# Optimization experiments

Hardware: AMD Instinct MI355X
Metric: run time of the kernel (lower is better)

## Reference

```python
import jax, jax.numpy as jnp
import numpy as np

EPS = 1e-6

def _phi(x):
    # elu(x) + 1 feature map
    return jax.nn.elu(x) + 1.0

def setup_inputs() -> dict:
    key = jax.random.key(0)
    kq, kk, kv = jax.random.split(key, 3)
    N, L, S, H, D, M = 8, 4096, 4096, 8, 64, 64
    queries = jax.random.normal(kq, (N, L, H, D), dtype=jnp.float32)
    keys = jax.random.normal(kk, (N, S, H, D), dtype=jnp.float32)
    values = jax.random.normal(kv, (N, S, H, M), dtype=jnp.float32)
    key_mask = jnp.ones((N, S), dtype=jnp.float32)  # key_lengths.float_matrix
    return {"queries": queries, "keys": keys, "values": values, "key_mask": key_mask}

def reference(queries, keys, values, key_mask):
    Q = _phi(queries)                                   # [N,L,H,D]
    K = _phi(keys) * key_mask[:, :, None, None]         # [N,S,H,D]
    KV = jnp.einsum('nshd,nshm->nhmd', K, values)       # [N,H,M,D]
    Z = 1.0 / (jnp.einsum('nlhd,nhd->nlh', Q, K.sum(axis=1)) + EPS)  # [N,L,H]
    V = jnp.einsum('nlhd,nhmd,nlh->nlhm', Q, KV, Z)     # [N,L,H,M]
    return V
```

## Files before the change

### kernel.cpp

```cpp
#include <hip/hip_runtime.h>


#define SLEN 4096
#define LLEN 4096
#define NHTOT 64
#define HD   512
#define NSPLIT 8
#define EPSF 1e-6f

typedef short s16x8 __attribute__((ext_vector_type(8)));
typedef float f32x4 __attribute__((ext_vector_type(4)));

__device__ __forceinline__ float phi(float x) {
    return x > 0.0f ? x + 1.0f : __expf(x);
}

__device__ __forceinline__ unsigned pack_hi2(float a, float b) {
    return (__float_as_uint(a) >> 16) | (__float_as_uint(b) & 0xFFFF0000u);
}
__device__ __forceinline__ float bres(float x) {
    return x - __uint_as_float(__float_as_uint(x) & 0xFFFF0000u);
}
__device__ __forceinline__ void bsplit(float x, short& hi, short& lo) {
    const unsigned bx = __float_as_uint(x);
    hi = (short)(bx >> 16);
    const float hf = __uint_as_float(bx & 0xFFFF0000u);
    lo = (short)(__float_as_uint(x - hf) >> 16);
}

__global__ __launch_bounds__(256, 2)
void la_phase1(const float* __restrict__ Kg, const float* __restrict__ Vg,
               const float* __restrict__ maskg,
               float* __restrict__ KVp, float* __restrict__ Ksump) {
    __shared__ float smem[4][4096];
    __shared__ float ksb[16 * 64];

    const int tid  = threadIdx.x;
    const int w    = tid >> 6;
    const int lane = tid & 63;
    const int nh   = blockIdx.y;
    const int n    = nh >> 3;
    const int h    = nh & 7;
    const int sp   = blockIdx.x;

    const int r  = lane & 15;
    const int a  = lane >> 4;
    const int c4 = r * 4;

    char* const wbase = (char*)&smem[w][0];
    char* const kthi = wbase;
    char* const ktlo = wbase + 4096;
    char* const vthi = wbase + 8192;
    char* const vtlo = wbase + 12288;

    const size_t base = (size_t)n * SLEN * HD + (size_t)h * 64;
    const float* mrow = maskg + (size_t)n * SLEN;
    const int wrow0 = sp * 512 + w * 128;

    const int woff0 = ((((a >> 1) ^ (r & 3)) << 4) | ((a & 1) << 3));
    const int rkey  = (r >> 2) & 3;

    f32x4 acc[4][4];
    #pragma unroll
    for (int i = 0; i < 4; ++i)
        #pragma unroll
        for (int j = 0; j < 4; ++j)
            acc[i][j] = (f32x4){0.f, 0.f, 0.f, 0.f};
    float4 ksp = make_float4(0.f, 0.f, 0.f, 0.f);

    float4 pk[2][4], pv[2][4];
    float  pm[2][4];
    #pragma unroll
    for (int u = 0; u < 2; ++u)
        #pragma unroll
        for (int j = 0; j < 4; ++j) {
            const int s = wrow0 + u * 16 + a * 4 + j;
            const size_t g = base + (size_t)s * HD + c4;
            pk[u][j] = *(const float4*)(Kg + g);
            pv[u][j] = *(const float4*)(Vg + g);
            pm[u][j] = mrow[s];
        }

    #pragma unroll
    for (int t = 0; t < 4; ++t) {
        #pragma unroll
        for (int u = 0; u < 2; ++u) {
            float4 kf[4];
            #pragma unroll
            for (int j = 0; j < 4; ++j) {
                float4 kq = pk[u][j];
                const float mm = pm[u][j];
                kq.x = phi(kq.x) * mm; kq.y = phi(kq.y) * mm;
                kq.z = phi(kq.z) * mm; kq.w = phi(kq.w) * mm;
                kf[j] = kq;
                ksp.x += kq.x; ksp.y += kq.y; ksp.z += kq.z; ksp.w += kq.w;
            }
            const int wo = woff0 ^ (u << 5);
            #pragma unroll
            for (int i = 0; i < 4; ++i) {
                const int doff = r * 256 + i * 64 + wo;
                const float k0 = (&kf[0].x)[i], k1 = (&kf[1].x)[i];
                const float k2 = (&kf[2].x)[i], k3 = (&kf[3].x)[i];
                *(uint2*)(kthi + doff) = make_uint2(pack_hi2(k0, k1), pack_hi2(k2, k3));
                *(uint2*)(ktlo + doff) = make_uint2(pack_hi2(bres(k0), bres(k1)),
                                                   pack_hi2(bres(k2), bres(k3)));
                const float v0 = (&pv[u][0].x)[i], v1 = (&pv[u][1].x)[i];
                const float v2 = (&pv[u][2].x)[i], v3 = (&pv[u][3].x)[i];
                *(uint2*)(vthi + doff) = make_uint2(pack_hi2(v0, v1), pack_hi2(v2, v3));
                *(uint2*)(vtlo + doff) = make_uint2(pack_hi2(bres(v0), bres(v1)),
                                                   pack_hi2(bres(v2), bres(v3)));
            }
        }
        if (t < 3) {
            #pragma unroll
            for (int u = 0; u < 2; ++u)
                #pragma unroll
                for (int j = 0; j < 4; ++j) {
                    const int s = wrow0 + (t + 1) * 32 + u * 16 + a * 4 + j;
                    const size_t g = base + (size_t)s * HD + c4;
                    pk[u][j] = *(const float4*)(Kg + g);
                    pv[u][j] = *(const float4*)(Vg + g);
                    pm[u][j] = mrow[s];
                }
        }
        s16x8 Ah[4], Al[4];
        const int cho = (a ^ rkey) << 4;
        #pragma unroll
        for (int dt = 0; dt < 4; ++dt) {
            const int off = dt * 1024 + r * 64 + cho;
            Ah[dt] = *(const s16x8*)(kthi + off);
            Al[dt] = *(const s16x8*)(ktlo + off);
        }
        #pragma unroll
        for (int mt = 0; mt < 4; ++mt) {
            const int off = mt * 1024 + r * 64 + cho;
            const s16x8 Bh = *(const s16x8*)(vthi + off);
            const s16x8 Bl = *(const s16x8*)(vtlo + off);
            #pragma unroll
            for (int dt = 0; dt < 4; ++dt) {
                acc[dt][mt] = __builtin_amdgcn_mfma_f32_16x16x32_bf16(Ah[dt], Bh, acc[dt][mt], 0, 0, 0);
                acc[dt][mt] = __builtin_amdgcn_mfma_f32_16x16x32_bf16(Ah[dt], Bl, acc[dt][mt], 0, 0, 0);
                acc[dt][mt] = __builtin_amdgcn_mfma_f32_16x16x32_bf16(Al[dt], Bh, acc[dt][mt], 0, 0, 0);
            }
        }
    }

    *(float4*)&ksb[(w * 4 + a) * 64 + c4] = ksp;

    float* pw = &smem[w][0];
    #pragma unroll
    for (int dt = 0; dt < 4; ++dt)
        #pragma unroll
        for (int mt = 0; mt < 4; ++mt)
            #pragma unroll
            for (int p = 0; p < 4; ++p)
                pw[(dt * 16 + a * 4 + p) * 64 + mt * 16 + r] = acc[dt][mt][p];
    __syncthreads();

    float* outp = KVp + ((size_t)sp * NHTOT + nh) * 4096;
    #pragma unroll
    for (int j = 0; j < 4; ++j) {
        const int f = (j * 256 + tid) * 4;
        float4 s0  = *(const float4*)&smem[0][f];
        const float4 b1 = *(const float4*)&smem[1][f];
        const float4 b2 = *(const float4*)&smem[2][f];
        const float4 b3 = *(const float4*)&smem[3][f];
        s0.x += b1.x + b2.x + b3.x;
        s0.y += b1.y + b2.y + b3.y;
        s0.z += b1.z + b2.z + b3.z;
        s0.w += b1.w + b2.w + b3.w;
        *(float4*)&outp[f] = s0;
    }
    if (tid < 64) {
        float ssum = 0.f;
        #pragma unroll
        for (int rr = 0; rr < 16; ++rr) ssum += ksb[rr * 64 + tid];
        Ksump[((size_t)sp * NHTOT + nh) * 64 + tid] = ssum;
    }
}

__global__ __launch_bounds__(256)
void la_reduce(const float* __restrict__ KVp, const float* __restrict__ Ksump,
               short* __restrict__ KVThi, short* __restrict__ KVTlo,
               float* __restrict__ Ksum) {
    __shared__ float ld[64 * 20];

    const int nh  = blockIdx.y;
    const int mb  = blockIdx.x * 16;
    const int tid = threadIdx.x;

    const int d    = tid >> 2;
    const int moff = (tid & 3) * 4;
    float4 a = make_float4(0.f, 0.f, 0.f, 0.f);
    #pragma unroll
    for (int s = 0; s < NSPLIT; ++s) {
        const float4 v = *(const float4*)&KVp[((size_t)s * NHTOT + nh) * 4096 + d * 64 + mb + moff];
        a.x += v.x; a.y += v.y; a.z += v.z; a.w += v.w;
    }
    *(float4*)&ld[d * 20 + moff] = a;
    __syncthreads();

    const int mloc = tid >> 4;
    const int d0   = (tid & 15) * 4;
    short hi4[4], lo4[4];
    #pragma unroll
    for (int i = 0; i < 4; ++i)
        bsplit(ld[(d0 + i) * 20 + mloc], hi4[i], lo4[i]);
    const size_t o = (size_t)nh * 4096 + (mb + mloc) * 64 + d0;
    *(short4*)&KVThi[o] = *(short4*)hi4;
    *(short4*)&KVTlo[o] = *(short4*)lo4;

    if (blockIdx.x == 0 && tid < 64) {
        float b = 0.f;
        #pragma unroll
        for (int s = 0; s < NSPLIT; ++s)
            b += Ksump[((size_t)s * NHTOT + nh) * 64 + tid];
        Ksum[nh * 64 + tid] = b;
    }
}

__global__ __launch_bounds__(256)
void la_phase2(const float* __restrict__ Qg,
               const short* __restrict__ KVThi, const short* __restrict__ KVTlo,
               const float* __restrict__ Ksum, float* __restrict__ Og) {
    const int tid  = threadIdx.x;
    const int w    = tid >> 6;
    const int lane = tid & 63;
    const int nh   = blockIdx.y;
    const int n    = nh >> 3;
    const int h    = nh & 7;
    const int l0   = blockIdx.x * 128 + w * 32;

    const int r  = lane & 15;
    const int g4 = lane >> 4;

    const short* bhp = KVThi + (size_t)nh * 4096;
    const short* blp = KVTlo + (size_t)nh * 4096;
    const float* ksp = Ksum + nh * 64;

    f32x4 acc[2][4];
    #pragma unroll
    for (int t = 0; t < 2; ++t)
        #pragma unroll
        for (int u = 0; u < 4; ++u)
            acc[t][u] = (f32x4){0.f, 0.f, 0.f, 0.f};
    float den[2] = {0.f, 0.f};

    #pragma unroll
    for (int g = 0; g < 2; ++g) {
        const int db = g * 32 + g4 * 8;

        s16x8 Bh[4], Bl[4];
        #pragma unroll
        for (int u = 0; u < 4; ++u) {
            Bh[u] = *(const s16x8*)&bhp[(u * 16 + r) * 64 + db];
            Bl[u] = *(const s16x8*)&blp[(u * 16 + r) * 64 + db];
        }
        const float4 k0 = *(const float4*)&ksp[db];
        const float4 k1 = *(const float4*)&ksp[db + 4];

        #pragma unroll
        for (int t = 0; t < 2; ++t) {
            const float* qrow = Qg + ((size_t)(n * LLEN + l0 + t * 16 + r) * 8 + h) * 64 + db;
            float4 q0 = *(const float4*)qrow;
            float4 q1 = *(const float4*)(qrow + 4);
            q0.x = phi(q0.x); q0.y = phi(q0.y); q0.z = phi(q0.z); q0.w = phi(q0.w);
            q1.x = phi(q1.x); q1.y = phi(q1.y); q1.z = phi(q1.z); q1.w = phi(q1.w);

            float dn = den[t];
            dn = fmaf(q0.x, k0.x, dn); dn = fmaf(q0.y, k0.y, dn);
            dn = fmaf(q0.z, k0.z, dn); dn = fmaf(q0.w, k0.w, dn);
            dn = fmaf(q1.x, k1.x, dn); dn = fmaf(q1.y, k1.y, dn);
            dn = fmaf(q1.z, k1.z, dn); dn = fmaf(q1.w, k1.w, dn);
            den[t] = dn;

            s16x8 Ah, Al;
            {
                short hh, ll;
                bsplit(q0.x, hh, ll); Ah[0] = hh; Al[0] = ll;
                bsplit(q0.y, hh, ll); Ah[1] = hh; Al[1] = ll;
                bsplit(q0.z, hh, ll); Ah[2] = hh; Al[2] = ll;
                bsplit(q0.w, hh, ll); Ah[3] = hh; Al[3] = ll;
                bsplit(q1.x, hh, ll); Ah[4] = hh; Al[4] = ll;
                bsplit(q1.y, hh, ll); Ah[5] = hh; Al[5] = ll;
                bsplit(q1.z, hh, ll); Ah[6] = hh; Al[6] = ll;
                bsplit(q1.w, hh, ll); Ah[7] = hh; Al[7] = ll;
            }
            #pragma unroll
            for (int u = 0; u < 4; ++u) {
                acc[t][u] = __builtin_amdgcn_mfma_f32_16x16x32_bf16(Ah, Bh[u], acc[t][u], 0, 0, 0);
                acc[t][u] = __builtin_amdgcn_mfma_f32_16x16x32_bf16(Ah, Bl[u], acc[t][u], 0, 0, 0);
                acc[t][u] = __builtin_amdgcn_mfma_f32_16x16x32_bf16(Al, Bh[u], acc[t][u], 0, 0, 0);
            }
        }
    }

    #pragma unroll
    for (int t = 0; t < 2; ++t) {
        den[t] += __shfl_xor(den[t], 16, 64);
        den[t] += __shfl_xor(den[t], 32, 64);
    }

    #pragma unroll
    for (int t = 0; t < 2; ++t) {
        #pragma unroll
        for (int k = 0; k < 4; ++k) {
            const int ro = g4 * 4 + k;
            const float dk = __shfl(den[t], ro, 64);
            const float z  = 1.0f / (dk + EPSF);
            const int l = l0 + t * 16 + ro;
            float* op = &Og[((size_t)(n * LLEN + l) * 8 + h) * 64 + r];
            #pragma unroll
            for (int u = 0; u < 4; ++u)
                op[u * 16] = acc[t][u][k] * z;
        }
    }
}

extern "C" void kernel_launch(void* const* d_in, const int* in_sizes, int n_in,
                              void* d_out, int out_size, void* d_ws, size_t ws_size,
                              hipStream_t stream) {
    const float* Q    = (const float*)d_in[0];
    const float* K    = (const float*)d_in[1];
    const float* V    = (const float*)d_in[2];
    const float* mask = (const float*)d_in[3];
    float* out = (float*)d_out;

    float* KVp   = (float*)d_ws;
    float* Ksump = KVp + (size_t)NSPLIT * NHTOT * 4096;
    float* Ksum  = Ksump + (size_t)NSPLIT * NHTOT * 64;
    short* KVThi = (short*)(Ksum + NHTOT * 64);
    short* KVTlo = KVThi + (size_t)NHTOT * 4096;

    dim3 g1(NSPLIT, NHTOT);
    la_phase1<<<g1, 256, 0, stream>>>(K, V, mask, KVp, Ksump);

    dim3 gr(4, NHTOT);
    la_reduce<<<gr, 256, 0, stream>>>(KVp, Ksump, KVThi, KVTlo, Ksum);

    dim3 g2(LLEN / 128, NHTOT);
    la_phase2<<<g2, 256, 0, stream>>>(Q, KVThi, KVTlo, Ksum, out);
}
```

Baseline: 239.3 us.

## Restructure phase1 into shared-tile 2x2 warp MFMA split with double-buffered LDS

Phase 1 now has the block cooperatively stage a 32-row K/V tile into double-buffered shared memory. Two waves convert K and two convert V, and each wave computes a 32x32 quadrant of the 64x64 KV product instead of a full 64x64 partial over its own rows. This removes the per-wave partial-sum reduction through shared memory, cuts LDS use and accumulator registers, and allows four blocks per CU. In exchange it doubles NSPLIT to 16, which adds partial-sum traffic for the reduce kernel, and it adds a barrier on every iteration.

```diff
diff --git a/kernel.cpp b/kernel.cpp
--- a/kernel.cpp
+++ b/kernel.cpp
@@ -5,7 +5,7 @@
 #define LLEN 4096
 #define NHTOT 64
 #define HD   512
-#define NSPLIT 8
+#define NSPLIT 16
 #define EPSF 1e-6f
 
 typedef short s16x8 __attribute__((ext_vector_type(8)));
@@ -28,12 +28,12 @@
     lo = (short)(__float_as_uint(x - hf) >> 16);
 }
 
-__global__ __launch_bounds__(256, 2)
+__global__ __launch_bounds__(256, 4)
 void la_phase1(const float* __restrict__ Kg, const float* __restrict__ Vg,
                const float* __restrict__ maskg,
                float* __restrict__ KVp, float* __restrict__ Ksump) {
-    __shared__ float smem[4][4096];
-    __shared__ float ksb[16 * 64];
+    __shared__ char  sb[2][16384];
+    __shared__ float ksb[8 * 64];
 
     const int tid  = threadIdx.x;
     const int w    = tid >> 6;
@@ -43,140 +43,120 @@
     const int h    = nh & 7;
     const int sp   = blockIdx.x;
 
-    const int r  = lane & 15;
-    const int a  = lane >> 4;
-    const int c4 = r * 4;
-
-    char* const wbase = (char*)&smem[w][0];
-    char* const kthi = wbase;
-    char* const ktlo = wbase + 4096;
-    char* const vthi = wbase + 8192;
-    char* const vtlo = wbase + 12288;
+    const bool isK = (w < 2);
+    const int idx  = tid & 127;
+    const int c    = idx & 15;
+    const int q    = idx >> 4;
+    const int c4   = c * 4;
+    const float* __restrict__ src = isK ? Kg : Vg;
+    const int arro = isK ? 0 : 8192;
+    const int woff = (((q >> 1) ^ (c & 3)) << 4) | ((q & 1) << 3);
+
+    const int wd = w & 1, wm = w >> 1;
+    const int r  = lane & 15, a = lane >> 4;
+    const int cho = ((a ^ ((r >> 2) & 3)) << 4);
 
     const size_t base = (size_t)n * SLEN * HD + (size_t)h * 64;
     const float* mrow = maskg + (size_t)n * SLEN;
-    const int wrow0 = sp * 512 + w * 128;
-
-    const int woff0 = ((((a >> 1) ^ (r & 3)) << 4) | ((a & 1) << 3));
-    const int rkey  = (r >> 2) & 3;
-
-    f32x4 acc[4][4];
-    #pragma unroll
-    for (int i = 0; i < 4; ++i)
-        #pragma unroll
-        for (int j = 0; j < 4; ++j)
-            acc[i][j] = (f32x4){0.f, 0.f, 0.f, 0.f};
+    const int brow0 = sp * 256;
+
+    f32x4 acc[2][2];
+    #pragma unroll
+    for (int dt = 0; dt < 2; ++dt)
+        #pragma unroll
+        for (int mt = 0; mt < 2; ++mt)
+            acc[dt][mt] = (f32x4){0.f, 0.f, 0.f, 0.f};
     float4 ksp = make_float4(0.f, 0.f, 0.f, 0.f);
 
-    float4 pk[2][4], pv[2][4];
-    float  pm[2][4];
-    #pragma unroll
-    for (int u = 0; u < 2; ++u)
-        #pragma unroll
-        for (int j = 0; j < 4; ++j) {
-            const int s = wrow0 + u * 16 + a * 4 + j;
-            const size_t g = base + (size_t)s * HD + c4;
-            pk[u][j] = *(const float4*)(Kg + g);
-            pv[u][j] = *(const float4*)(Vg + g);
-            pm[u][j] = mrow[s];
-        }
-
-    #pragma unroll
-    for (int t = 0; t < 4; ++t) {
-        #pragma unroll
-        for (int u = 0; u < 2; ++u) {
-            float4 kf[4];
+    float4 p[4];
+    float  pm[4];
+    #pragma unroll
+    for (int j = 0; j < 4; ++j) {
+        const int s = brow0 + q * 4 + j;
+        p[j] = *(const float4*)(src + base + (size_t)s * HD + c4);
+        if (isK) pm[j] = mrow[s];
+    }
+
+    #pragma unroll 2
+    for (int t = 0; t < 8; ++t) {
+        char* bb = &sb[t & 1][arro];
+        float4 vv[4];
+        if (isK) {
             #pragma unroll
             for (int j = 0; j < 4; ++j) {
-                float4 kq = pk[u][j];
-                const float mm = pm[u][j];
+                float4 kq = p[j];
+                const float mm = pm[j];
                 kq.x = phi(kq.x) * mm; kq.y = phi(kq.y) * mm;
                 kq.z = phi(kq.z) * mm; kq.w = phi(kq.w) * mm;
-                kf[j] = kq;
                 ksp.x += kq.x; ksp.y += kq.y; ksp.z += kq.z; ksp.w += kq.w;
-            }
-            const int wo = woff0 ^ (u << 5);
-            #pragma unroll
-            for (int i = 0; i < 4; ++i) {
-                const int doff = r * 256 + i * 64 + wo;
-                const float k0 = (&kf[0].x)[i], k1 = (&kf[1].x)[i];
-                const float k2 = (&kf[2].x)[i], k3 = (&kf[3].x)[i];
-                *(uint2*)(kthi + doff) = make_uint2(pack_hi2(k0, k1), pack_hi2(k2, k3));
-                *(uint2*)(ktlo + doff) = make_uint2(pack_hi2(bres(k0), bres(k1)),
-                                                   pack_hi2(bres(k2), bres(k3)));
-                const float v0 = (&pv[u][0].x)[i], v1 = (&pv[u][1].x)[i];
-                const float v2 = (&pv[u][2].x)[i], v3 = (&pv[u][3].x)[i];
-                *(uint2*)(vthi + doff) = make_uint2(pack_hi2(v0, v1), pack_hi2(v2, v3));
-                *(uint2*)(vtlo + doff) = make_uint2(pack_hi2(bres(v0), bres(v1)),
-                                                   pack_hi2(bres(v2), bres(v3)));
-            }
-        }
-        if (t < 3) {
-            #pragma unroll
-            for (int u = 0; u < 2; ++u)
-                #pragma unroll
-                for (int j = 0; j < 4; ++j) {
-                    const int s = wrow0 + (t + 1) * 32 + u * 16 + a * 4 + j;
-                    const size_t g = base + (size_t)s * HD + c4;
-                    pk[u][j] = *(const float4*)(Kg + g);
-                    pv[u][j] = *(const float4*)(Vg + g);
-                    pm[u][j] = mrow[s];
-                }
-        }
-        s16x8 Ah[4], Al[4];
-        const int cho = (a ^ rkey) << 4;
-        #pragma unroll
-        for (int dt = 0; dt < 4; ++dt) {
-            const int off = dt * 1024 + r * 64 + cho;
-            Ah[dt] = *(const s16x8*)(kthi + off);
-            Al[dt] = *(const s16x8*)(ktlo + off);
-        }
-        #pragma unroll
-        for (int mt = 0; mt < 4; ++mt) {
-            const int off = mt * 1024 + r * 64 + cho;
-            const s16x8 Bh = *(const s16x8*)(vthi + off);
-            const s16x8 Bl = *(const s16x8*)(vtlo + off);
-            #pragma unroll
-            for (int dt = 0; dt < 4; ++dt) {
-                acc[dt][mt] = __builtin_amdgcn_mfma_f32_16x16x32_bf16(Ah[dt], Bh, acc[dt][mt], 0, 0, 0);
-                acc[dt][mt] = __builtin_amdgcn_mfma_f32_16x16x32_bf16(Ah[dt], Bl, acc[dt][mt], 0, 0, 0);
-                acc[dt][mt] = __builtin_amdgcn_mfma_f32_16x16x32_bf16(Al[dt], Bh, acc[dt][mt], 0, 0, 0);
-            }
-        }
-    }
-
-    *(float4*)&ksb[(w * 4 + a) * 64 + c4] = ksp;
-
-    float* pw = &smem[w][0];
-    #pragma unroll
-    for (int dt = 0; dt < 4; ++dt)
-        #pragma unroll
-        for (int mt = 0; mt < 4; ++mt)
-            #pragma unroll
-            for (int p = 0; p < 4; ++p)
-                pw[(dt * 16 + a * 4 + p) * 64 + mt * 16 + r] = acc[dt][mt][p];
+                vv[j] = kq;
+            }
+        } else {
+            #pragma unroll
+            for (int j = 0; j < 4; ++j) vv[j] = p[j];
+        }
+        #pragma unroll
+        for (int i = 0; i < 4; ++i) {
+            const int doff = (c4 + i) * 64 + woff;
+            const float x0 = (&vv[0].x)[i], x1 = (&vv[1].x)[i];
+            const float x2 = (&vv[2].x)[i], x3 = (&vv[3].x)[i];
+            *(uint2*)(bb + doff)        = make_uint2(pack_hi2(x0, x1), pack_hi2(x2, x3));
+            *(uint2*)(bb + 4096 + doff) = make_uint2(pack_hi2(bres(x0), bres(x1)),
+                                                     pack_hi2(bres(x2), bres(x3)));
+        }
+        __syncthreads();
+
+        if (t < 7) {
+            #pragma unroll
+            for (int j = 0; j < 4; ++j) {
+                const int s = brow0 + (t + 1) * 32 + q * 4 + j;
+                p[j] = *(const float4*)(src + base + (size_t)s * HD + c4);
+                if (isK) pm[j] = mrow[s];
+            }
+        }
+
+        const char* rbK = &sb[t & 1][0];
+        const char* rbV = &sb[t & 1][8192];
+        s16x8 Ah[2], Al[2], Bh[2], Bl[2];
+        #pragma unroll
+        for (int dt = 0; dt < 2; ++dt) {
+            const int off = ((wd * 2 + dt) * 16 + r) * 64 + cho;
+            Ah[dt] = *(const s16x8*)(rbK + off);
+            Al[dt] = *(const s16x8*)(rbK + 4096 + off);
+        }
+        #pragma unroll
+        for (int mt = 0; mt < 2; ++mt) {
+            const int off = ((wm * 2 + mt) * 16 + r) * 64 + cho;
+            Bh[mt] = *(const s16x8*)(rbV + off);
+            Bl[mt] = *(const s16x8*)(rbV + 4096 + off);
+        }
+        #pragma unroll
+        for (int dt = 0; dt < 2; ++dt)
+            #pragma unroll
+            for (int mt = 0; mt < 2; ++mt) {
+                acc[dt][mt] = __builtin_amdgcn_mfma_f32_16x16x32_bf16(Ah[dt], Bh[mt], acc[dt][mt], 0, 0, 0);
+                acc[dt][mt] = __builtin_amdgcn_mfma_f32_16x16x32_bf16(Ah[dt], Bl[mt], acc[dt][mt], 0, 0, 0);
+                acc[dt][mt] = __builtin_amdgcn_mfma_f32_16x16x32_bf16(Al[dt], Bh[mt], acc[dt][mt], 0, 0, 0);
+            }
+    }
+
+    if (isK) *(float4*)&ksb[q * 64 + c4] = ksp;
     __syncthreads();
-
-    float* outp = KVp + ((size_t)sp * NHTOT + nh) * 4096;
-    #pragma unroll
-    for (int j = 0; j < 4; ++j) {
-        const int f = (j * 256 + tid) * 4;
-        float4 s0  = *(const float4*)&smem[0][f];
-        const float4 b1 = *(const float4*)&smem[1][f];
-        const float4 b2 = *(const float4*)&smem[2][f];
-        const float4 b3 = *(const float4*)&smem[3][f];
-        s0.x += b1.x + b2.x + b3.x;
-        s0.y += b1.y + b2.y + b3.y;
-        s0.z += b1.z + b2.z + b3.z;
-        s0.w += b1.w + b2.w + b3.w;
-        *(float4*)&outp[f] = s0;
-    }
     if (tid < 64) {
         float ssum = 0.f;
         #pragma unroll
-        for (int rr = 0; rr < 16; ++rr) ssum += ksb[rr * 64 + tid];
+        for (int rr = 0; rr < 8; ++rr) ssum += ksb[rr * 64 + tid];
         Ksump[((size_t)sp * NHTOT + nh) * 64 + tid] = ssum;
     }
+
+    float* outp = KVp + ((size_t)sp * NHTOT + nh) * 4096;
+    #pragma unroll
+    for (int dt = 0; dt < 2; ++dt)
+        #pragma unroll
+        for (int mt = 0; mt < 2; ++mt)
+            #pragma unroll
+            for (int pp = 0; pp < 4; ++pp)
+                outp[(wd * 32 + dt * 16 + a * 4 + pp) * 64 + wm * 32 + mt * 16 + r] = acc[dt][mt][pp];
 }
 
 __global__ __launch_bounds__(256)
```

New measurement: 244.6 us. +2.2%, slower.
